# Optimization experiments

Measured on AMD Instinct MI355X. Metric: run time of the kernel, lower is better.

Reference implementation:

```python
import jax, jax.numpy as jnp
import numpy as np

STRIDE = 32
ANCHORS = np.array([[10, 13], [16, 30], [33, 23], [30, 61], [62, 45],
                    [59, 119], [116, 90], [156, 198], [373, 326]], np.float32)
ALL_ANCH = ANCHORS / STRIDE           # [9,2] anchor w,h in grid units
ANCH_MASK = [6, 7, 8]
MASKED_ANCH = ALL_ANCH[ANCH_MASK]     # [3,2]
N_CLASSES = 80
N_ANCHORS = 3
IGNORE_THRE = 0.5


def _bce_sum(p, t, w=1.0):
    # torch BCELoss(sum): clamps log terms at -100 to avoid 0*inf
    lp = jnp.maximum(jnp.log(p), -100.0)
    lq = jnp.maximum(jnp.log(1.0 - p), -100.0)
    return jnp.sum(-w * (t * lp + (1.0 - t) * lq))


def _iou_xywh(a, b):
    # a: [B,N,4], b: [B,K,4] in (cx,cy,w,h) -> IoU [B,N,K]
    tl = jnp.maximum(a[:, :, None, :2] - a[:, :, None, 2:] / 2,
                     b[:, None, :, :2] - b[:, None, :, 2:] / 2)
    br = jnp.minimum(a[:, :, None, :2] + a[:, :, None, 2:] / 2,
                     b[:, None, :, :2] + b[:, None, :, 2:] / 2)
    en = jnp.all(tl < br, axis=-1).astype(a.dtype)
    inter = jnp.prod(br - tl, axis=-1) * en
    area_a = a[:, :, 2] * a[:, :, 3]
    area_b = b[:, :, 2] * b[:, :, 3]
    return inter / (area_a[:, :, None] + area_b[:, None, :] - inter)


def setup_inputs() -> dict:
    key = jax.random.key(0)
    k1, k2, k3, k4 = jax.random.split(key, 4)
    B, M, F, A, NC = 128, 60, 19, 3, 80
    output = jax.random.normal(k1, (B, A * (5 + NC), F, F), jnp.float32)
    cxy = jax.random.uniform(k2, (B, M, 2), jnp.float32, 100.0, 500.0)
    wh = jax.random.uniform(k3, (B, M, 2), jnp.float32, 64.0, 192.0)
    cls = jax.random.randint(k4, (B, M, 1), 0, NC).astype(jnp.float32)
    labels = jnp.concatenate([cxy - wh / 2, cxy + wh / 2, cls], axis=-1)
    return {"output": output, "labels": labels}


def reference(output, labels):
    B = output.shape[0]
    F = output.shape[2]
    n_ch = 5 + N_CLASSES
    labels = jax.lax.stop_gradient(labels)  # torch detaches labels

    # [B, A, F, F, n_ch]; sigmoid on x,y,obj,cls; raw on w,h
    out = output.reshape(B, N_ANCHORS, n_ch, F, F).transpose(0, 1, 3, 4, 2)
    out = jnp.concatenate([jax.nn.sigmoid(out[..., :2]), out[..., 2:4],
                           jax.nn.sigmoid(out[..., 4:])], axis=-1)

    # decoded pred boxes (grid units), detached as in torch (.data)
    xs = jnp.arange(F, dtype=out.dtype)
    wa = jnp.asarray(MASKED_ANCH[:, 0])[None, :, None, None]
    ha = jnp.asarray(MASKED_ANCH[:, 1])[None, :, None, None]
    px = out[..., 0] + xs[None, None, None, :]
    py = out[..., 1] + xs[None, None, :, None]
    pw = jnp.exp(out[..., 2]) * wa
    ph = jnp.exp(out[..., 3]) * ha
    pred = jax.lax.stop_gradient(jnp.stack([px, py, pw, ph], axis=-1))

    valid = labels.sum(axis=2) > 0                               # [B,M]
    tx = jnp.floor(labels[..., 0] / STRIDE)
    ty = jnp.floor(labels[..., 1] / STRIDE)
    tw = jnp.floor((labels[..., 2] - labels[..., 0]) / STRIDE)
    th = jnp.floor((labels[..., 3] - labels[..., 1]) / STRIDE)
    ti = tx.astype(jnp.int32)
    tj = ty.astype(jnp.int32)

    # anchor matching: IoU of (0,0,w,h) truths vs (0,0,aw,ah) ref anchors
    ref_wh = jnp.asarray(ALL_ANCH)                               # [9,2]
    mw = jnp.minimum(tw[..., None], ref_wh[:, 0])
    mh = jnp.minimum(th[..., None], ref_wh[:, 1])
    en = ((mw > 0) & (mh > 0)).astype(out.dtype)
    inter = mw * mh * en
    aiou = inter / (tw[..., None] * th[..., None]
                    + ref_wh[:, 0] * ref_wh[:, 1] - inter)       # [B,M,9]
    best_all = jnp.argmax(aiou, axis=-1)                         # [B,M]
    best_n = best_all % 3
    best_mask = best_all >= ANCH_MASK[0]

    # ignore mask from pred-vs-truth IoU
    truth_box = jnp.stack([tx, ty, tw, th], axis=-1)             # [B,M,4]
    ious = _iou_xywh(pred.reshape(B, -1, 4), truth_box)          # [B,AFF,M]
    ious = ious * valid[:, None, :].astype(out.dtype)
    best_iou = ious.max(axis=-1)
    obj_mask = (best_iou <= IGNORE_THRE).astype(out.dtype).reshape(B, N_ANCHORS, F, F)

    # scatter matched truths into (b, a, j, i) cells
    matched = valid & best_mask                                  # [B,M]
    NT = B * N_ANCHORS * F * F
    b_idx = jnp.broadcast_to(jnp.arange(B, dtype=jnp.int32)[:, None], matched.shape)
    flat = ((b_idx * N_ANCHORS + best_n.astype(jnp.int32)) * F + tj) * F + ti
    flat = jnp.where(matched, flat, NT).reshape(-1)              # NT is OOB -> dropped

    obj_mask = obj_mask.reshape(-1).at[flat].set(1.0, mode='drop').reshape(B, N_ANCHORS, F, F)
    tgt_mask = jnp.zeros((NT, 4 + N_CLASSES), out.dtype).at[flat].set(1.0, mode='drop')
    tgt_mask = tgt_mask.reshape(B, N_ANCHORS, F, F, 4 + N_CLASSES)

    txf = tx - tx.astype(jnp.int32).astype(out.dtype)   # exactly 0 (as in torch)
    tyf = ty - ty.astype(jnp.int32).astype(out.dtype)
    anch = jnp.asarray(MASKED_ANCH)[best_n]                      # [B,M,2]
    twt = jnp.log(tw / anch[..., 0] + 1e-16)
    tht = jnp.log(th / anch[..., 1] + 1e-16)
    onehot = jax.nn.one_hot(labels[..., 4].astype(jnp.int32), N_CLASSES, dtype=out.dtype)
    trow = jnp.concatenate([txf[..., None], tyf[..., None], twt[..., None],
                            tht[..., None], jnp.ones_like(txf)[..., None],
                            onehot], axis=-1).reshape(-1, n_ch)
    target = jnp.zeros((NT, n_ch), out.dtype).at[flat].set(trow, mode='drop')
    target = target.reshape(B, N_ANCHORS, F, F, n_ch)

    scale_val = jnp.sqrt(2.0 - tw * th / (F * F))                # [B,M]
    srow = jnp.broadcast_to(scale_val[..., None], scale_val.shape + (2,)).reshape(-1, 2)
    tgt_scale = jnp.zeros((NT, 2), out.dtype).at[flat].set(srow, mode='drop')
    tgt_scale = tgt_scale.reshape(B, N_ANCHORS, F, F, 2)

    # apply masks (in-place multiplies in torch)
    out_xy = out[..., :2] * tgt_mask[..., :2]
    out_wh = out[..., 2:4] * tgt_mask[..., 2:4] * tgt_scale
    out_obj = out[..., 4] * obj_mask
    out_cls = out[..., 5:] * tgt_mask[..., 4:]
    tgt_xy = target[..., :2] * tgt_mask[..., :2]
    tgt_wh = target[..., 2:4] * tgt_mask[..., 2:4] * tgt_scale
    tgt_obj = target[..., 4] * obj_mask
    tgt_cls = target[..., 5:] * tgt_mask[..., 4:]

    loss_xy = _bce_sum(out_xy, tgt_xy, tgt_scale * tgt_scale)
    loss_wh = 0.5 * jnp.sum((out_wh - tgt_wh) ** 2)
    loss_obj = _bce_sum(out_obj, tgt_obj)
    loss_cls = _bce_sum(out_cls, tgt_cls)
    out_full = jnp.concatenate([out_xy, out_wh, out_obj[..., None], out_cls], axis=-1)
    tgt_full = jnp.concatenate([tgt_xy, tgt_wh, tgt_obj[..., None], tgt_cls], axis=-1)
    loss_l2 = jnp.sum((out_full - tgt_full) ** 2)
    loss = loss_xy + loss_wh + loss_obj + loss_cls
    return (loss, loss_xy, loss_wh, loss_obj, loss_cls, loss_l2)
```

## Files before the change

### kernel.cpp

```cpp
#include <hip/hip_runtime.h>

#define NB 128
#define NM 60
#define NF 19
#define NA 3
#define NCELL (NF*NF)
#define NCH 85
#define NCHTOT (NA*NCH)
#define TPB 192
#define NWAVE (TPB/64)

__device__ __constant__ float c_aw[9] = {0.3125f, 0.5f, 1.03125f, 0.9375f, 1.9375f, 1.84375f, 3.625f, 4.875f, 11.65625f};
__device__ __constant__ float c_ah[9] = {0.40625f, 0.9375f, 0.71875f, 1.90625f, 1.40625f, 3.71875f, 2.8125f, 6.1875f, 10.1875f};

__device__ __forceinline__ float clog(float v) { return fmaxf(__logf(v), -100.0f); }
__device__ __forceinline__ float sigm(float x) { return 1.0f / (1.0f + __expf(-x)); }

__device__ __forceinline__ float wave_sum(float v) {
    for (int off = 32; off > 0; off >>= 1) v += __shfl_down(v, off, 64);
    return v;
}

__global__ __launch_bounds__(TPB) void k_main(const float* __restrict__ out,
                                              const float* __restrict__ labels,
                                              float* __restrict__ res) {
    __shared__ float4 s_box[NM];
    __shared__ float  s_ar[NM];
    __shared__ float  s_scale[NM], s_twt[NM], s_tht[NM], s_txf[NM], s_tyf[NM];
    __shared__ int    s_cls[NM];
    __shared__ int    s_win[NCELL];
    __shared__ int    s_list[64];
    __shared__ int    s_n;
    __shared__ float  s_red[NWAVE][5];

    const int blk  = blockIdx.x;
    const int ba   = blk >> 1;
    const int half = blk & 1;
    const int b = ba / NA, a = ba % NA;
    const int tid = threadIdx.x;
    const int cell = half * TPB + tid;
    const bool active = cell < NCELL;

    const float* obase = out + ((size_t)b * NCHTOT + a * NCH) * NCELL;
    float r0 = 0.f, r1 = 0.f, r2 = 0.f, r3 = 0.f, r4 = 0.f;
    if (active) {
        r0 = obase[0 * NCELL + cell];
        r1 = obase[1 * NCELL + cell];
        r2 = obase[2 * NCELL + cell];
        r3 = obase[3 * NCELL + cell];
        r4 = obase[4 * NCELL + cell];
    }

    for (int c = tid; c < NCELL; c += TPB) s_win[c] = -1;
    if (tid == 0) s_n = 0;
    __syncthreads();

    if (tid < NM) {
        const float* l = labels + ((size_t)b * NM + tid) * 5;
        float x1 = l[0], y1 = l[1], x2 = l[2], y2 = l[3], cf = l[4];
        bool valid = (x1 + y1 + x2 + y2 + cf) > 0.0f;
        float tx = floorf(x1 * 0.03125f);
        float ty = floorf(y1 * 0.03125f);
        float tw = floorf((x2 - x1) * 0.03125f);
        float th = floorf((y2 - y1) * 0.03125f);
        int ti = (int)tx, tj = (int)ty;
        float bst = -1.0f; int bi = 0;
        #pragma unroll
        for (int q = 0; q < 9; q++) {
            float mw = fminf(tw, c_aw[q]), mh = fminf(th, c_ah[q]);
            float inter = (mw > 0.0f && mh > 0.0f) ? mw * mh : 0.0f;
            float iou = inter / (tw * th + c_aw[q] * c_ah[q] - inter);
            if (iou > bst) { bst = iou; bi = q; }
        }
        int bn = bi % 3;
        s_box[tid] = valid ? make_float4(tx - 0.5f * tw, ty - 0.5f * th,
                                         tx + 0.5f * tw, ty + 0.5f * th)
                           : make_float4(3.0e8f, 3.0e8f, 3.0e8f, 3.0e8f);
        s_ar[tid]    = tw * th;
        s_scale[tid] = sqrtf(2.0f - tw * th * (1.0f / (float)NCELL));
        s_twt[tid]   = __logf(tw / c_aw[6 + bn] + 1e-16f);
        s_tht[tid]   = __logf(th / c_ah[6 + bn] + 1e-16f);
        s_txf[tid]   = tx - (float)ti;
        s_tyf[tid]   = ty - (float)tj;
        s_cls[tid]   = (int)cf;
        if (valid && bi >= 6 && bn == a &&
            ti >= 0 && ti < NF && tj >= 0 && tj < NF) {
            atomicMax(&s_win[tj * NF + ti], tid);
        }
    }
    __syncthreads();

    int ii = cell % NF, jj = cell / NF;
    float sx = sigm(r0), sy = sigm(r1), sobj = sigm(r4);
    float pw = __expf(r2) * c_aw[6 + a], ph = __expf(r3) * c_ah[6 + a];
    float px = sx + (float)ii, py = sy + (float)jj;
    float px1 = px - 0.5f * pw, px2 = px + 0.5f * pw;
    float py1 = py - 0.5f * ph, py2 = py + 0.5f * ph;
    float parea = pw * ph;

    float best = 0.0f;
    #pragma unroll 4
    for (int m = 0; m < NM; m++) {
        float4 tb = s_box[m];
        float tlx = fmaxf(px1, tb.x), tly = fmaxf(py1, tb.y);
        float brx = fminf(px2, tb.z), bry = fminf(py2, tb.w);
        if (tlx < brx && tly < bry) {
            float inter = (brx - tlx) * (bry - tly);
            best = fmaxf(best, inter / (parea + s_ar[m] - inter));
        }
    }

    float lxy = 0.f, lwh = 0.f, lobj = 0.f, lcls = 0.f, ll2 = 0.f;
    int w = active ? s_win[cell] : -1;
    if (w >= 0) {
        float s = s_scale[w], s2 = s * s;
        float txf = s_txf[w], tyf = s_tyf[w];
        float dw = r2 - s_twt[w], dh = r3 - s_tht[w];
        lxy = -s2 * (txf * clog(sx) + (1.0f - txf) * clog(1.0f - sx)
                   + tyf * clog(sy) + (1.0f - tyf) * clog(1.0f - sy));
        float whsq = s2 * (dw * dw + dh * dh);
        lwh = 0.5f * whsq;
        lobj = -clog(sobj);
        ll2 = (sx - txf) * (sx - txf) + (sy - tyf) * (sy - tyf)
            + whsq + (sobj - 1.0f) * (sobj - 1.0f);
        int pos = atomicAdd(&s_n, 1);
        s_list[pos] = cell | (s_cls[w] << 16);
    } else if (active && best <= 0.5f) {
        lobj = -clog(1.0f - sobj);
        ll2 = sobj * sobj;
    }
    __syncthreads();

    int nlist = s_n;
    int lane = tid & 63, wid = tid >> 6;
    for (int e = wid; e < nlist; e += NWAVE) {
        int packed = s_list[e];
        int mc = packed & 0xFFFF, k = packed >> 16;
        const float* p = obase + (size_t)5 * NCELL + mc;
        {
            float sc = sigm(p[(size_t)lane * NCELL]);
            bool isk = (lane == k);
            lcls -= isk ? clog(sc) : clog(1.0f - sc);
            float d = isk ? (sc - 1.0f) : sc;
            ll2 += d * d;
        }
        if (lane < 16) {
            int c2 = lane + 64;
            float sc = sigm(p[(size_t)c2 * NCELL]);
            bool isk = (c2 == k);
            lcls -= isk ? clog(sc) : clog(1.0f - sc);
            float d = isk ? (sc - 1.0f) : sc;
            ll2 += d * d;
        }
    }

    float v0 = wave_sum(lxy), v1 = wave_sum(lwh), v2 = wave_sum(lobj);
    float v3 = wave_sum(lcls), v4 = wave_sum(ll2);
    if (lane == 0) {
        s_red[wid][0] = v0; s_red[wid][1] = v1; s_red[wid][2] = v2;
        s_red[wid][3] = v3; s_red[wid][4] = v4;
    }
    __syncthreads();
    if (tid < 5) {
        float s = 0.0f;
        for (int wv = 0; wv < NWAVE; wv++) s += s_red[wv][tid];
        atomicAdd(&res[tid + 1], s);
        if (tid < 4) atomicAdd(&res[0], s);
    }
}

extern "C" void kernel_launch(void* const* d_in, const int* in_sizes, int n_in,
                              void* d_out, int out_size, void* d_ws, size_t ws_size,
                              hipStream_t stream) {
    (void)in_sizes; (void)n_in; (void)out_size; (void)d_ws; (void)ws_size;
    const float* output = (const float*)d_in[0];
    const float* labels = (const float*)d_in[1];
    float* res = (float*)d_out;

    hipMemsetAsync(res, 0, 6 * sizeof(float), stream);
    k_main<<<NB * NA * 2, TPB, 0, stream>>>(output, labels, res);
}
```

Measured before the change: 113.8 us.

## Split IoU box loop across two thread groups and replace atomics with two-pass reduction

Doubles the block size so that two thread groups each handle half of the 60 ground-truth boxes in the ignore-mask IoU max loop, then merges the two partial maxima through shared memory. The IoU loop becomes branchless with a reciprocal in place of the division. One barrier is removed. Global float atomics and the memset are replaced by per-block partial sums written to workspace and a second single-block reduction kernel. This adds a second launch and doubles threads per block, and the final summation order changes.

```diff
diff --git a/kernel.cpp b/kernel.cpp
--- a/kernel.cpp
+++ b/kernel.cpp
@@ -7,8 +7,10 @@
 #define NCELL (NF*NF)
 #define NCH 85
 #define NCHTOT (NA*NCH)
-#define TPB 192
+#define HALFC 192
+#define TPB 384
 #define NWAVE (TPB/64)
+#define NBLK (NB*NA*2)
 
 __device__ __constant__ float c_aw[9] = {0.3125f, 0.5f, 1.03125f, 0.9375f, 1.9375f, 1.84375f, 3.625f, 4.875f, 11.65625f};
 __device__ __constant__ float c_ah[9] = {0.40625f, 0.9375f, 0.71875f, 1.90625f, 1.40625f, 3.71875f, 2.8125f, 6.1875f, 10.1875f};
@@ -23,12 +25,13 @@
 
 __global__ __launch_bounds__(TPB) void k_main(const float* __restrict__ out,
                                               const float* __restrict__ labels,
-                                              float* __restrict__ res) {
+                                              float* __restrict__ partial) {
     __shared__ float4 s_box[NM];
     __shared__ float  s_ar[NM];
     __shared__ float  s_scale[NM], s_twt[NM], s_tht[NM], s_txf[NM], s_tyf[NM];
     __shared__ int    s_cls[NM];
     __shared__ int    s_win[NCELL];
+    __shared__ float  s_hi[HALFC];
     __shared__ int    s_list[64];
     __shared__ int    s_n;
     __shared__ float  s_red[NWAVE][5];
@@ -38,7 +41,9 @@
     const int half = blk & 1;
     const int b = ba / NA, a = ba % NA;
     const int tid = threadIdx.x;
-    const int cell = half * TPB + tid;
+    const int grp   = (tid >= HALFC) ? 1 : 0;
+    const int local = tid - grp * HALFC;
+    const int cell  = half * HALFC + local;
     const bool active = cell < NCELL;
 
     const float* obase = out + ((size_t)b * NCHTOT + a * NCH) * NCELL;
@@ -48,12 +53,11 @@
         r1 = obase[1 * NCELL + cell];
         r2 = obase[2 * NCELL + cell];
         r3 = obase[3 * NCELL + cell];
-        r4 = obase[4 * NCELL + cell];
+        if (grp == 0) r4 = obase[4 * NCELL + cell];
     }
 
     for (int c = tid; c < NCELL; c += TPB) s_win[c] = -1;
     if (tid == 0) s_n = 0;
-    __syncthreads();
 
     if (tid < NM) {
         const float* l = labels + ((size_t)b * NM + tid) * 5;
@@ -99,35 +103,39 @@
     float parea = pw * ph;
 
     float best = 0.0f;
-    #pragma unroll 4
-    for (int m = 0; m < NM; m++) {
+    const int mstart = grp * (NM / 2);
+    #pragma unroll 5
+    for (int m = mstart; m < mstart + NM / 2; m++) {
         float4 tb = s_box[m];
-        float tlx = fmaxf(px1, tb.x), tly = fmaxf(py1, tb.y);
-        float brx = fminf(px2, tb.z), bry = fminf(py2, tb.w);
-        if (tlx < brx && tly < bry) {
-            float inter = (brx - tlx) * (bry - tly);
-            best = fmaxf(best, inter / (parea + s_ar[m] - inter));
-        }
-    }
+        float dx = fminf(px2, tb.z) - fmaxf(px1, tb.x);
+        float dy = fminf(py2, tb.w) - fmaxf(py1, tb.y);
+        float inter = fmaxf(dx, 0.0f) * fmaxf(dy, 0.0f);
+        best = fmaxf(best, inter * __frcp_rn(parea + s_ar[m] - inter));
+    }
+    if (grp == 1) s_hi[local] = best;
+    __syncthreads();
 
     float lxy = 0.f, lwh = 0.f, lobj = 0.f, lcls = 0.f, ll2 = 0.f;
-    int w = active ? s_win[cell] : -1;
-    if (w >= 0) {
-        float s = s_scale[w], s2 = s * s;
-        float txf = s_txf[w], tyf = s_tyf[w];
-        float dw = r2 - s_twt[w], dh = r3 - s_tht[w];
-        lxy = -s2 * (txf * clog(sx) + (1.0f - txf) * clog(1.0f - sx)
-                   + tyf * clog(sy) + (1.0f - tyf) * clog(1.0f - sy));
-        float whsq = s2 * (dw * dw + dh * dh);
-        lwh = 0.5f * whsq;
-        lobj = -clog(sobj);
-        ll2 = (sx - txf) * (sx - txf) + (sy - tyf) * (sy - tyf)
-            + whsq + (sobj - 1.0f) * (sobj - 1.0f);
-        int pos = atomicAdd(&s_n, 1);
-        s_list[pos] = cell | (s_cls[w] << 16);
-    } else if (active && best <= 0.5f) {
-        lobj = -clog(1.0f - sobj);
-        ll2 = sobj * sobj;
+    if (grp == 0 && active) {
+        best = fmaxf(best, s_hi[local]);
+        int w = s_win[cell];
+        if (w >= 0) {
+            float s = s_scale[w], s2 = s * s;
+            float txf = s_txf[w], tyf = s_tyf[w];
+            float dw = r2 - s_twt[w], dh = r3 - s_tht[w];
+            lxy = -s2 * (txf * clog(sx) + (1.0f - txf) * clog(1.0f - sx)
+                       + tyf * clog(sy) + (1.0f - tyf) * clog(1.0f - sy));
+            float whsq = s2 * (dw * dw + dh * dh);
+            lwh = 0.5f * whsq;
+            lobj = -clog(sobj);
+            ll2 = (sx - txf) * (sx - txf) + (sy - tyf) * (sy - tyf)
+                + whsq + (sobj - 1.0f) * (sobj - 1.0f);
+            int pos = atomicAdd(&s_n, 1);
+            s_list[pos] = cell | (s_cls[w] << 16);
+        } else if (best <= 0.5f) {
+            lobj = -clog(1.0f - sobj);
+            ll2 = sobj * sobj;
+        }
     }
     __syncthreads();
 
@@ -163,20 +171,49 @@
     __syncthreads();
     if (tid < 5) {
         float s = 0.0f;
+        #pragma unroll
         for (int wv = 0; wv < NWAVE; wv++) s += s_red[wv][tid];
-        atomicAdd(&res[tid + 1], s);
-        if (tid < 4) atomicAdd(&res[0], s);
+        partial[(size_t)blk * 5 + tid] = s;
+    }
+}
+
+__global__ __launch_bounds__(256) void k_reduce(const float* __restrict__ partial,
+                                                float* __restrict__ res) {
+    __shared__ float s[4][5];
+    int tid = threadIdx.x;
+    float acc[5] = {0.f, 0.f, 0.f, 0.f, 0.f};
+    for (int i = tid; i < NBLK; i += 256) {
+        const float* p = partial + (size_t)i * 5;
+        acc[0] += p[0]; acc[1] += p[1]; acc[2] += p[2];
+        acc[3] += p[3]; acc[4] += p[4];
+    }
+    #pragma unroll
+    for (int j = 0; j < 5; j++) acc[j] = wave_sum(acc[j]);
+    int lane = tid & 63, wid = tid >> 6;
+    if (lane == 0) {
+        #pragma unroll
+        for (int j = 0; j < 5; j++) s[wid][j] = acc[j];
+    }
+    __syncthreads();
+    if (tid == 0) {
+        float t[5];
+        #pragma unroll
+        for (int j = 0; j < 5; j++) t[j] = s[0][j] + s[1][j] + s[2][j] + s[3][j];
+        res[0] = t[0] + t[1] + t[2] + t[3];
+        res[1] = t[0]; res[2] = t[1]; res[3] = t[2];
+        res[4] = t[3]; res[5] = t[4];
     }
 }
 
 extern "C" void kernel_launch(void* const* d_in, const int* in_sizes, int n_in,
                               void* d_out, int out_size, void* d_ws, size_t ws_size,
                               hipStream_t stream) {
-    (void)in_sizes; (void)n_in; (void)out_size; (void)d_ws; (void)ws_size;
+    (void)in_sizes; (void)n_in; (void)out_size; (void)ws_size;
     const float* output = (const float*)d_in[0];
     const float* labels = (const float*)d_in[1];
     float* res = (float*)d_out;
-
-    hipMemsetAsync(res, 0, 6 * sizeof(float), stream);
-    k_main<<<NB * NA * 2, TPB, 0, stream>>>(output, labels, res);
-}
+    float* partial = (float*)d_ws;
+
+    k_main<<<NBLK, TPB, 0, stream>>>(output, labels, partial);
+    k_reduce<<<1, 256, 0, stream>>>(partial, res);
+}
```

After: 96.96 us. 14.8% less time.
